# Optimization experiments

Measured on AMD Instinct MI355X. Metric: run time of the kernel, lower is better.

Reference implementation:

```python
import jax, jax.numpy as jnp
import numpy as np

N = 100000
E = 1600000
IN_F = 256
OUT_F = 128
ALPHA = 0.2  # LeakyReLU negative slope


def setup_inputs() -> dict:
    key = jax.random.key(0)
    k_x, k_e, k_w, k_al, k_ar = jax.random.split(key, 5)
    x = jax.random.normal(k_x, (N, IN_F), dtype=jnp.float32)
    edge_index = jax.random.randint(k_e, (2, E), 0, N, dtype=jnp.int64)
    # xavier_uniform with gain=1.414
    gain = 1.414
    lim_w = gain * np.sqrt(6.0 / (IN_F + OUT_F))
    W = jax.random.uniform(k_w, (IN_F, OUT_F), dtype=jnp.float32, minval=-lim_w, maxval=lim_w)
    lim_a = gain * np.sqrt(6.0 / (OUT_F + 1))
    a_left = jax.random.uniform(k_al, (OUT_F, 1), dtype=jnp.float32, minval=-lim_a, maxval=lim_a)
    a_right = jax.random.uniform(k_ar, (OUT_F, 1), dtype=jnp.float32, minval=-lim_a, maxval=lim_a)
    return {"x": x, "edge_index": edge_index, "W": W, "a_left": a_left, "a_right": a_right}


def reference(x, edge_index, W, a_left, a_right):
    src = edge_index[0]  # destination of aggregation (rows of adj)
    dst = edge_index[1]  # neighbor being attended to
    Wh = x @ W                              # [N, out_f]
    e_left = (Wh @ a_left)[:, 0]            # [N]
    e_right = (Wh @ a_right)[:, 0]          # [N]
    e = e_left[src] + e_right[dst]          # [E]
    e = jnp.where(e > 0, e, ALPHA * e)      # LeakyReLU
    # segment softmax over edges grouped by src node
    e_max = jax.ops.segment_max(e, src, num_segments=N)          # [N]
    e_exp = jnp.exp(e - e_max[src])                               # [E]
    e_sum = jax.ops.segment_sum(e_exp, src, num_segments=N)       # [N]
    alpha = e_exp / (e_sum[src] + 1e-9)                           # [E]
    messages = alpha[:, None] * Wh[dst]                           # [E, out_f]
    output = jax.ops.segment_sum(messages, src, num_segments=N)   # [N, out_f]
    return jax.nn.relu(output)
```

## Files before the change

### kernel.cpp

```cpp
#include <hip/hip_runtime.h>
#include <cstdint>
#include <cstddef>

static constexpr int IN_F  = 256;
static constexpr int OUT_F = 128;
#define ALPHA_SLOPE 0.2f
#define NB 256
#define BUCK_SH 7
#define CAP 6144

typedef __attribute__((ext_vector_type(8))) short short8;
typedef __attribute__((ext_vector_type(4))) float f32x4;
union ABFrag { uint32_t u[4]; short8 v; };

#define AS1 __attribute__((address_space(1)))
#define AS3 __attribute__((address_space(3)))

__device__ __forceinline__ uint32_t pack_bf2(float lo, float hi) {
    uint32_t ul = __float_as_uint(lo), uh = __float_as_uint(hi);
    uint32_t rl = (ul + 0x7fffu + ((ul >> 16) & 1u)) >> 16;
    uint32_t rh = (uh + 0x7fffu + ((uh >> 16) & 1u)) & 0xffff0000u;
    return rl | rh;
}
__device__ __forceinline__ uint32_t cvtpk_bf2(float lo, float hi) {
    uint32_t r;
    asm("v_cvt_pk_bf16_f32 %0, %1, %2" : "=v"(r) : "v"(lo), "v"(hi));
    return r;
}
__device__ __forceinline__ float blo(uint32_t w) { return __uint_as_float(w << 16); }
__device__ __forceinline__ float bhi(uint32_t w) { return __uint_as_float(w & 0xffff0000u); }

#define RL_F(x, l) __uint_as_float(__builtin_amdgcn_readlane(__float_as_uint(x), (l)))
#define RL_I(x, l) __builtin_amdgcn_readlane((x), (l))

__device__ __forceinline__ int edge_at(const void* ei, int idx, int is64) {
    return is64 ? (int)((const long long*)ei)[idx] : ((const int*)ei)[idx];
}

__global__ __launch_bounds__(256) void prep_hist_kernel(
    const float* __restrict__ W, const float* __restrict__ aL,
    const float* __restrict__ aR, const void* __restrict__ EI,
    int E, int nbuk, uint32_t* __restrict__ WtH,
    float* __restrict__ waL, float* __restrict__ waR, int* __restrict__ C)
{
    if (blockIdx.x < 64) {
        int dd = blockIdx.x * 256 + threadIdx.x;
        int n  = dd >> 7;
        int kd = (dd & 127) ^ ((n & 7) << 2);
        int k  = kd * 2;
        WtH[dd] = pack_bf2(W[(size_t)k * OUT_F + n], W[(size_t)(k + 1) * OUT_F + n]);
        return;
    }
    if (blockIdx.x == 64) {
        int k = threadIdx.x;
        const float* wr = W + (size_t)k * OUT_F;
        float sl = 0.f, sr = 0.f;
        for (int j = 0; j < OUT_F; j++) {
            float wv = wr[j];
            sl = fmaf(wv, aL[j], sl);
            sr = fmaf(wv, aR[j], sr);
        }
        waL[k] = sl; waR[k] = sr;
        return;
    }
    __shared__ int h[800];
    __shared__ int det;
    if (threadIdx.x == 0) det = 0;
    for (int b = threadIdx.x; b < nbuk; b += 256) h[b] = 0;
    __syncthreads();
    {
        const unsigned* eu = (const unsigned*)EI;
        int nz = 0;
        for (int i = threadIdx.x; i < 1024; i += 256)
            if (eu[2 * i + 1] != 0u) nz++;
        if (nz) atomicAdd(&det, 1);
    }
    __syncthreads();
    const int is64 = (det == 0);
    const int bid = blockIdx.x - 65;
    int chunk = (E + NB - 1) / NB;
    int start = bid * chunk;
    int end = min(start + chunk, E);
    for (int i = start + threadIdx.x; i < end; i += 256) {
        int s = edge_at(EI, i, is64);
        atomicAdd(&h[s >> BUCK_SH], 1);
    }
    __syncthreads();
    for (int b = threadIdx.x; b < nbuk; b += 256)
        C[b * NB + bid] = h[b];
}

__global__ __launch_bounds__(256) void scan1_kernel(const int* __restrict__ counts,
                                                    int* __restrict__ offsets,
                                                    int* __restrict__ partials, int N) {
    __shared__ int wt[4];
    int gid = blockIdx.x * 256 + threadIdx.x;
    const int lane = threadIdx.x & 63, wave = threadIdx.x >> 6;
    int c = (gid < N) ? counts[gid] : 0;
    int incl = c;
#pragma unroll
    for (int o = 1; o < 64; o <<= 1) {
        int v = __shfl_up(incl, o);
        if (lane >= o) incl += v;
    }
    if (lane == 63) wt[wave] = incl;
    __syncthreads();
    int woff = 0;
    for (int w = 0; w < wave; w++) woff += wt[w];
    if (gid < N) offsets[gid] = woff + incl - c;
    if (threadIdx.x == 0) partials[blockIdx.x] = wt[0] + wt[1] + wt[2] + wt[3];
}

__global__ __launch_bounds__(256) void scan2_kernel(int* data, int n) {
    __shared__ int wt[4];
    __shared__ int carry_s;
    if (threadIdx.x == 0) carry_s = 0;
    __syncthreads();
    const int lane = threadIdx.x & 63, wave = threadIdx.x >> 6;
    for (int base = 0; base < n; base += 256) {
        int i = base + threadIdx.x;
        int c = (i < n) ? data[i] : 0;
        int incl = c;
#pragma unroll
        for (int o = 1; o < 64; o <<= 1) {
            int v = __shfl_up(incl, o);
            if (lane >= o) incl += v;
        }
        if (lane == 63) wt[wave] = incl;
        __syncthreads();
        int woff = 0;
        for (int w = 0; w < wave; w++) woff += wt[w];
        int total = wt[0] + wt[1] + wt[2] + wt[3];
        int carry = carry_s;
        __syncthreads();
        if (i < n) data[i] = carry + woff + incl - c;
        if (threadIdx.x == 0) carry_s = carry + total;
        __syncthreads();
    }
}

__global__ __launch_bounds__(512, 4) void gemm_scatter_kernel(
    const float* __restrict__ X, const uint32_t* __restrict__ WtH,
    const float* __restrict__ waL, const float* __restrict__ waR,
    uint32_t* __restrict__ Whh, float* __restrict__ el, float* __restrict__ er,
    int M, const void* __restrict__ EI, int E, int nbuk,
    const int* __restrict__ Cx, const int* __restrict__ T,
    uint32_t* __restrict__ entries, int GB)
{
    __shared__ uint32_t ldsW[16384];
    __shared__ float    ldsWA[512];
    __shared__ int cur[800];
    __shared__ int det;
    const int tid = threadIdx.x;

    if (blockIdx.x >= GB) {
        if (tid == 0) det = 0;
        for (int b = tid; b < nbuk; b += 512) cur[b] = 0;
        __syncthreads();
        {
            const unsigned* eu = (const unsigned*)EI;
            int nz = 0;
            for (int i = tid; i < 1024; i += 512)
                if (eu[2 * i + 1] != 0u) nz++;
            if (nz) atomicAdd(&det, 1);
        }
        __syncthreads();
        const int is64 = (det == 0);
        const int bid = blockIdx.x - GB;
        int chunk = (E + NB - 1) / NB;
        int start = bid * chunk;
        int end = min(start + chunk, E);
        for (int i = start + tid; i < end; i += 512) {
            int s = edge_at(EI, i, is64);
            int d = edge_at(EI, E + i, is64);
            int b = s >> BUCK_SH;
            int pos = T[b] + Cx[b * NB + bid] + atomicAdd(&cur[b], 1);
            entries[pos] = ((uint32_t)(s & 127) << 17) | (uint32_t)d;
        }
        return;
    }

    const int w = tid >> 6, l = tid & 63;
    const int c = l & 15, kg = l >> 4;
    const int swz = (c & 7) << 2;

    const int bm = blockIdx.x * 128;
    const int myrow = w * 16 + c;
    const int grow = min(bm + myrow, M - 1);
    const bool rv = (bm + myrow) < M;
    const float* xp = X + (size_t)grow * IN_F + kg * 8;

    {
        const float* wsrc = (tid < 256) ? (waL + tid) : (waR + (tid - 256));
        __builtin_amdgcn_global_load_lds((AS1 const void*)wsrc,
                                         (AS3 void*)&ldsWA[tid], 4, 0, 0);
    }
    {
        const uint4* wsrc = (const uint4*)WtH;
        uint4* wdst = (uint4*)ldsW;
#pragma unroll
        for (int i = 0; i < 8; i++)
            __builtin_amdgcn_global_load_lds((AS1 const void*)(wsrc + tid + i * 512),
                                             (AS3 void*)(wdst + tid + i * 512), 16, 0, 0);
    }
    __builtin_amdgcn_sched_barrier(0);

    f32x4 xv[16];
#define GLOAD(DST, OFFS) \
    asm volatile("global_load_dwordx4 %0, %1, off offset:" OFFS : "=v"(DST) : "v"(xp))
    GLOAD(xv[0],  "0");   GLOAD(xv[1],  "16");
    GLOAD(xv[2],  "128"); GLOAD(xv[3],  "144");
    GLOAD(xv[4],  "256"); GLOAD(xv[5],  "272");
    GLOAD(xv[6],  "384"); GLOAD(xv[7],  "400");
    GLOAD(xv[8],  "512"); GLOAD(xv[9],  "528");
    GLOAD(xv[10], "640"); GLOAD(xv[11], "656");
    GLOAD(xv[12], "768"); GLOAD(xv[13], "784");
    GLOAD(xv[14], "896"); GLOAD(xv[15], "912");
#undef GLOAD
    __builtin_amdgcn_sched_barrier(0);

    f32x4 acc[8];
#pragma unroll
    for (int j = 0; j < 8; j++) acc[j] = (f32x4){0.f, 0.f, 0.f, 0.f};
    float sl = 0.f, sr = 0.f;

    asm volatile("s_waitcnt vmcnt(16)");
    __builtin_amdgcn_sched_barrier(0);
    __builtin_amdgcn_s_barrier();
    __builtin_amdgcn_sched_barrier(0);

#define GSTEP(KS, VMS)                                                        \
    {                                                                         \
        asm volatile("s_waitcnt vmcnt(" VMS ")");                             \
        __builtin_amdgcn_sched_barrier(0);                                    \
        f32x4 xa = xv[2 * KS], xb = xv[2 * KS + 1];                           \
        f32x4 l0 = *(const f32x4*)&ldsWA[KS * 32 + kg * 8];                   \
        f32x4 l1 = *(const f32x4*)&ldsWA[KS * 32 + kg * 8 + 4];               \
        f32x4 r0 = *(const f32x4*)&ldsWA[256 + KS * 32 + kg * 8];             \
        f32x4 r1 = *(const f32x4*)&ldsWA[256 + KS * 32 + kg * 8 + 4];         \
        _Pragma("unroll")                                                     \
        for (int i = 0; i < 4; i++) {                                         \
            sl = fmaf(xa[i], l0[i], sl); sl = fmaf(xb[i], l1[i], sl);         \
            sr = fmaf(xa[i], r0[i], sr); sr = fmaf(xb[i], r1[i], sr);         \
        }                                                                     \
        ABFrag a;                                                             \
        a.u[0] = cvtpk_bf2(xa[0], xa[1]); a.u[1] = cvtpk_bf2(xa[2], xa[3]);   \
        a.u[2] = cvtpk_bf2(xb[0], xb[1]); a.u[3] = cvtpk_bf2(xb[2], xb[3]);   \
        const int kd = KS * 16 + kg * 4;                                      \
        _Pragma("unroll")                                                     \
        for (int j = 0; j < 8; j++) {                                         \
            const int col = j * 16 + c;                                       \
            ABFrag b;                                                         \
            *(uint4*)b.u = *(const uint4*)&ldsW[col * 128 + (kd ^ swz)];      \
            acc[j] = __builtin_amdgcn_mfma_f32_16x16x32_bf16(a.v, b.v, acc[j], 0, 0, 0); \
        }                                                                     \
    }
    GSTEP(0, "14"); GSTEP(1, "12"); GSTEP(2, "10"); GSTEP(3, "8");
    GSTEP(4, "6");  GSTEP(5, "4");  GSTEP(6, "2");  GSTEP(7, "0");
#undef GSTEP

    sl += __shfl_xor(sl, 16); sl += __shfl_xor(sl, 32);
    sr += __shfl_xor(sr, 16); sr += __shfl_xor(sr, 32);
    if (rv && kg == 0) { el[bm + myrow] = sl; er[bm + myrow] = sr; }

    __syncthreads();
    float* sc = (float*)ldsW + w * 2048;
#pragma unroll
    for (int j = 0; j < 8; j++)
#pragma unroll
        for (int r = 0; r < 4; r++)
            sc[(kg * 4 + r) * 128 + j * 16 + c] = acc[j][r];
    __syncthreads();
#pragma unroll
    for (int m = 0; m < 16; m++) {
        float2 p = *(const float2*)&sc[m * 128 + 2 * l];
        int orow = bm + w * 16 + m;
        if (orow < M) Whh[(size_t)orow * 64 + l] = cvtpk_bf2(p.x, p.y);
    }
}

__global__ __launch_bounds__(256) void bucket_kernel(const uint32_t* __restrict__ entries,
                                                     const int* __restrict__ T,
                                                     int E, int N, int nbuk,
                                                     int* __restrict__ offsets,
                                                     int* __restrict__ edge_dst) {
    __shared__ uint32_t ent[CAP];
    __shared__ int outD[CAP];
    __shared__ int cnt[128], pre[128], cur[128];
    __shared__ int wt4[2];
    const int b = blockIdx.x;
    const int tid = threadIdx.x;
    const int base = T[b];
    const int cend = (b + 1 < nbuk) ? T[b + 1] : E;
    int count = cend - base;
    if (count > CAP) count = CAP;

    if (tid < 128) { cnt[tid] = 0; cur[tid] = 0; }
    __syncthreads();
    for (int k = tid; k < count; k += 256) {
        uint32_t e = entries[base + k];
        ent[k] = e;
        atomicAdd(&cnt[e >> 17], 1);
    }
    __syncthreads();
    {
        const int lane = tid & 63, w = tid >> 6;
        int c = (tid < 128) ? cnt[tid] : 0;
        int incl = c;
#pragma unroll
        for (int o = 1; o < 64; o <<= 1) {
            int v = __shfl_up(incl, o);
            if (lane >= o) incl += v;
        }
        if (w == 0 && lane == 63) wt4[0] = incl;
        __syncthreads();
        if (tid < 128) pre[tid] = ((w == 1) ? wt4[0] : 0) + incl - c;
        __syncthreads();
    }
    const int node0 = b << BUCK_SH;
    const int nnode = min(128, N - node0);
    if (tid < nnode) offsets[node0 + tid] = base + pre[tid];
    if (b == nbuk - 1 && tid == 0) offsets[N] = E;
    for (int k = tid; k < count; k += 256) {
        uint32_t e = ent[k];
        int sl = e >> 17;
        int p = pre[sl] + atomicAdd(&cur[sl], 1);
        outD[p] = (int)(e & 0x1FFFFu);
    }
    __syncthreads();
    for (int k = tid; k < count; k += 256)
        edge_dst[base + k] = outD[k];
}

__global__ __launch_bounds__(256) void node_kernel(const int* __restrict__ offsets,
                                                   const int* __restrict__ edge_dst,
                                                   const float* __restrict__ el,
                                                   const float* __restrict__ er,
                                                   const uint32_t* __restrict__ WhH,
                                                   float* __restrict__ out, int N) {
    int node = blockIdx.x * 4 + (threadIdx.x >> 6);
    int lane = threadIdx.x & 63;
    if (node >= N) return;
    int s0  = offsets[node];
    int deg = offsets[node + 1] - s0;
    float eli = el[node];

    if (deg <= 64) {
        int dj = 0;
        float e = -3.402823466e38f;
        if (lane < deg) {
            dj = edge_dst[s0 + lane];
            float t = eli + er[dj];
            e = t > 0.f ? t : ALPHA_SLOPE * t;
        }
        float m = e;
#pragma unroll
        for (int o = 32; o > 0; o >>= 1) m = fmaxf(m, __shfl_xor(m, o));
        float ex = (lane < deg) ? expf(e - m) : 0.f;
        float ssum = ex;
#pragma unroll
        for (int o = 32; o > 0; o >>= 1) ssum += __shfl_xor(ssum, o);
        float p = ex / (ssum + 1e-9f);

        const int g = lane >> 4, q = lane & 15;
        float a0 = 0.f, a1 = 0.f, a2 = 0.f, a3 = 0.f;
        float a4 = 0.f, a5 = 0.f, a6 = 0.f, a7 = 0.f;
        int rounds = (deg + 3) >> 2;
        int r = 0;
        for (; r + 4 <= rounds; r += 4) {
            int i0 = (r << 2) + g, i1 = i0 + 4, i2 = i0 + 8, i3 = i0 + 12;
            float p0 = __shfl(p, i0), p1 = __shfl(p, i1);
            float p2 = __shfl(p, i2), p3 = __shfl(p, i3);
            int   e0 = __shfl(dj, i0), e1 = __shfl(dj, i1);
            int   e2 = __shfl(dj, i2), e3 = __shfl(dj, i3);
            uint4 w0 = *(const uint4*)&WhH[(size_t)e0 * 64 + q * 4];
            uint4 w1 = *(const uint4*)&WhH[(size_t)e1 * 64 + q * 4];
            uint4 w2 = *(const uint4*)&WhH[(size_t)e2 * 64 + q * 4];
            uint4 w3 = *(const uint4*)&WhH[(size_t)e3 * 64 + q * 4];
            a0 = fmaf(p0, blo(w0.x), a0); a1 = fmaf(p0, bhi(w0.x), a1);
            a2 = fmaf(p0, blo(w0.y), a2); a3 = fmaf(p0, bhi(w0.y), a3);
            a4 = fmaf(p0, blo(w0.z), a4); a5 = fmaf(p0, bhi(w0.z), a5);
            a6 = fmaf(p0, blo(w0.w), a6); a7 = fmaf(p0, bhi(w0.w), a7);
            a0 = fmaf(p1, blo(w1.x), a0); a1 = fmaf(p1, bhi(w1.x), a1);
            a2 = fmaf(p1, blo(w1.y), a2); a3 = fmaf(p1, bhi(w1.y), a3);
            a4 = fmaf(p1, blo(w1.z), a4); a5 = fmaf(p1, bhi(w1.z), a5);
            a6 = fmaf(p1, blo(w1.w), a6); a7 = fmaf(p1, bhi(w1.w), a7);
            a0 = fmaf(p2, blo(w2.x), a0); a1 = fmaf(p2, bhi(w2.x), a1);
            a2 = fmaf(p2, blo(w2.y), a2); a3 = fmaf(p2, bhi(w2.y), a3);
            a4 = fmaf(p2, blo(w2.z), a4); a5 = fmaf(p2, bhi(w2.z), a5);
            a6 = fmaf(p2, blo(w2.w), a6); a7 = fmaf(p2, bhi(w2.w), a7);
            a0 = fmaf(p3, blo(w3.x), a0); a1 = fmaf(p3, bhi(w3.x), a1);
            a2 = fmaf(p3, blo(w3.y), a2); a3 = fmaf(p3, bhi(w3.y), a3);
            a4 = fmaf(p3, blo(w3.z), a4); a5 = fmaf(p3, bhi(w3.z), a5);
            a6 = fmaf(p3, blo(w3.w), a6); a7 = fmaf(p3, bhi(w3.w), a7);
        }
        for (; r + 2 <= rounds; r += 2) {
            int i0 = (r << 2) + g, i1 = i0 + 4;
            float p0 = __shfl(p, i0), p1 = __shfl(p, i1);
            int   e0 = __shfl(dj, i0), e1 = __shfl(dj, i1);
            uint4 w0 = *(const uint4*)&WhH[(size_t)e0 * 64 + q * 4];
            uint4 w1 = *(const uint4*)&WhH[(size_t)e1 * 64 + q * 4];
            a0 = fmaf(p0, blo(w0.x), a0); a1 = fmaf(p0, bhi(w0.x), a1);
            a2 = fmaf(p0, blo(w0.y), a2); a3 = fmaf(p0, bhi(w0.y), a3);
            a4 = fmaf(p0, blo(w0.z), a4); a5 = fmaf(p0, bhi(w0.z), a5);
            a6 = fmaf(p0, blo(w0.w), a6); a7 = fmaf(p0, bhi(w0.w), a7);
            a0 = fmaf(p1, blo(w1.x), a0); a1 = fmaf(p1, bhi(w1.x), a1);
            a2 = fmaf(p1, blo(w1.y), a2); a3 = fmaf(p1, bhi(w1.y), a3);
            a4 = fmaf(p1, blo(w1.z), a4); a5 = fmaf(p1, bhi(w1.z), a5);
            a6 = fmaf(p1, blo(w1.w), a6); a7 = fmaf(p1, bhi(w1.w), a7);
        }
        if (r < rounds) {
            int i0 = (r << 2) + g;
            float p0 = __shfl(p, i0);
            int   e0 = __shfl(dj, i0);
            uint4 w0 = *(const uint4*)&WhH[(size_t)e0 * 64 + q * 4];
            a0 = fmaf(p0, blo(w0.x), a0); a1 = fmaf(p0, bhi(w0.x), a1);
            a2 = fmaf(p0, blo(w0.y), a2); a3 = fmaf(p0, bhi(w0.y), a3);
            a4 = fmaf(p0, blo(w0.z), a4); a5 = fmaf(p0, bhi(w0.z), a5);
            a6 = fmaf(p0, blo(w0.w), a6); a7 = fmaf(p0, bhi(w0.w), a7);
        }
#pragma unroll
        for (int o = 16; o <= 32; o <<= 1) {
            a0 += __shfl_xor(a0, o); a1 += __shfl_xor(a1, o);
            a2 += __shfl_xor(a2, o); a3 += __shfl_xor(a3, o);
            a4 += __shfl_xor(a4, o); a5 += __shfl_xor(a5, o);
            a6 += __shfl_xor(a6, o); a7 += __shfl_xor(a7, o);
        }
        if (g == 0) {
            float4 o0 = make_float4(fmaxf(a0, 0.f), fmaxf(a1, 0.f),
                                    fmaxf(a2, 0.f), fmaxf(a3, 0.f));
            float4 o1 = make_float4(fmaxf(a4, 0.f), fmaxf(a5, 0.f),
                                    fmaxf(a6, 0.f), fmaxf(a7, 0.f));
            float* op = out + (size_t)node * OUT_F + q * 8;
            *(float4*)op = o0;
            *(float4*)(op + 4) = o1;
        }
        return;
    }

    float m = -3.402823466e38f;
    for (int j = lane; j < deg; j += 64) {
        float e = eli + er[edge_dst[s0 + j]];
        e = e > 0.f ? e : ALPHA_SLOPE * e;
        m = fmaxf(m, e);
    }
#pragma unroll
    for (int o = 32; o > 0; o >>= 1) m = fmaxf(m, __shfl_xor(m, o));

    float ssum = 0.f;
    for (int j = lane; j < deg; j += 64) {
        float e = eli + er[edge_dst[s0 + j]];
        e = e > 0.f ? e : ALPHA_SLOPE * e;
        ssum += expf(e - m);
    }
#pragma unroll
    for (int o = 32; o > 0; o >>= 1) ssum += __shfl_xor(ssum, o);
    float inv = 1.f / (ssum + 1e-9f);

    float acc0 = 0.f, acc1 = 0.f;
    for (int base = 0; base < deg; base += 64) {
        int j = base + lane;
        float p = 0.f;
        int d = 0;
        if (j < deg) {
            d = edge_dst[s0 + j];
            float e = eli + er[d];
            e = e > 0.f ? e : ALPHA_SLOPE * e;
            p = expf(e - m) * inv;
        }
        int cnt = min(64, deg - base);
        int t = 0;
        for (; t + 8 <= cnt; t += 8) {
            float b0 = RL_F(p, t + 0), b1 = RL_F(p, t + 1);
            float b2 = RL_F(p, t + 2), b3 = RL_F(p, t + 3);
            float b4 = RL_F(p, t + 4), b5 = RL_F(p, t + 5);
            float b6 = RL_F(p, t + 6), b7 = RL_F(p, t + 7);
            int   d0 = RL_I(d, t + 0), d1 = RL_I(d, t + 1);
            int   d2 = RL_I(d, t + 2), d3 = RL_I(d, t + 3);
            int   d4 = RL_I(d, t + 4), d5 = RL_I(d, t + 5);
            int   d6 = RL_I(d, t + 6), d7 = RL_I(d, t + 7);
            uint32_t w0 = WhH[(size_t)d0 * 64 + lane];
            uint32_t w1 = WhH[(size_t)d1 * 64 + lane];
            uint32_t w2 = WhH[(size_t)d2 * 64 + lane];
            uint32_t w3 = WhH[(size_t)d3 * 64 + lane];
            uint32_t w4 = WhH[(size_t)d4 * 64 + lane];
            uint32_t w5 = WhH[(size_t)d5 * 64 + lane];
            uint32_t w6 = WhH[(size_t)d6 * 64 + lane];
            uint32_t w7 = WhH[(size_t)d7 * 64 + lane];
            acc0 = fmaf(b0, blo(w0), acc0); acc1 = fmaf(b0, bhi(w0), acc1);
            acc0 = fmaf(b1, blo(w1), acc0); acc1 = fmaf(b1, bhi(w1), acc1);
            acc0 = fmaf(b2, blo(w2), acc0); acc1 = fmaf(b2, bhi(w2), acc1);
            acc0 = fmaf(b3, blo(w3), acc0); acc1 = fmaf(b3, bhi(w3), acc1);
            acc0 = fmaf(b4, blo(w4), acc0); acc1 = fmaf(b4, bhi(w4), acc1);
            acc0 = fmaf(b5, blo(w5), acc0); acc1 = fmaf(b5, bhi(w5), acc1);
            acc0 = fmaf(b6, blo(w6), acc0); acc1 = fmaf(b6, bhi(w6), acc1);
            acc0 = fmaf(b7, blo(w7), acc0); acc1 = fmaf(b7, bhi(w7), acc1);
        }
        for (; t < cnt; ++t) {
            float a = RL_F(p, t);
            int  dd = RL_I(d, t);
            uint32_t wv = WhH[(size_t)dd * 64 + lane];
            acc0 = fmaf(a, blo(wv), acc0);
            acc1 = fmaf(a, bhi(wv), acc1);
        }
    }
    out[(size_t)node * OUT_F + 2 * lane]     = fmaxf(acc0, 0.f);
    out[(size_t)node * OUT_F + 2 * lane + 1] = fmaxf(acc1, 0.f);
}

extern "C" void kernel_launch(void* const* d_in, const int* in_sizes, int n_in,
                              void* d_out, int out_size, void* d_ws, size_t ws_size,
                              hipStream_t stream) {
    (void)n_in; (void)out_size; (void)ws_size;
    const float* X  = (const float*)d_in[0];
    const void*  EI = d_in[1];
    const float* W  = (const float*)d_in[2];
    const float* aL = (const float*)d_in[3];
    const float* aR = (const float*)d_in[4];
    float* out = (float*)d_out;
    const int N = in_sizes[0] / IN_F;
    const int E = in_sizes[1] / 2;
    const int nbuk = (N + 127) >> BUCK_SH;
    const int GB = (N + 127) / 128;

    char* ws = (char*)d_ws;
    float*    waL      = (float*)(ws + 256);
    float*    waR      = waL + 256;
    uint32_t* WtH      = (uint32_t*)(waR + 256);
    uint32_t* Whh      = WtH + 16384;
    float*    el       = (float*)(Whh + (size_t)N * 64);
    float*    er       = el + N;
    int*      T        = (int*)(er + N);
    int*      C        = T + 1024;
    int*      Cx       = C + (size_t)nbuk * NB;
    int*      offsets  = Cx + (size_t)nbuk * NB;
    uint32_t* entries  = (uint32_t*)(offsets + (N + 1));
    int*      edge_dst = (int*)(entries + E);

    prep_hist_kernel<<<65 + NB, 256, 0, stream>>>(W, aL, aR, EI, E, nbuk,
                                                  WtH, waL, waR, C);
    scan1_kernel<<<nbuk, 256, 0, stream>>>(C, Cx, T, nbuk * NB);
    scan2_kernel<<<1, 256, 0, stream>>>(T, nbuk);
    gemm_scatter_kernel<<<GB + NB, 512, 0, stream>>>(X, WtH, waL, waR, Whh, el, er,
                                                     N, EI, E, nbuk, Cx, T,
                                                     entries, GB);
    bucket_kernel<<<nbuk, 256, 0, stream>>>(entries, T, E, N, nbuk, offsets, edge_dst);
    node_kernel<<<(N + 3) / 4, 256, 0, stream>>>(offsets, edge_dst, el, er, Whh, out, N);
}
```

Measured before the change: 151.7 us.

## Precast X to bf16 and compute attention logits in the scan kernel

```diff
diff --git a/kernel.cpp b/kernel.cpp
--- a/kernel.cpp
+++ b/kernel.cpp
@@ -90,25 +90,50 @@
         C[b * NB + bid] = h[b];
 }
 
-__global__ __launch_bounds__(256) void scan1_kernel(const int* __restrict__ counts,
-                                                    int* __restrict__ offsets,
-                                                    int* __restrict__ partials, int N) {
-    __shared__ int wt[4];
-    int gid = blockIdx.x * 256 + threadIdx.x;
-    const int lane = threadIdx.x & 63, wave = threadIdx.x >> 6;
-    int c = (gid < N) ? counts[gid] : 0;
-    int incl = c;
-#pragma unroll
-    for (int o = 1; o < 64; o <<= 1) {
-        int v = __shfl_up(incl, o);
-        if (lane >= o) incl += v;
-    }
-    if (lane == 63) wt[wave] = incl;
-    __syncthreads();
-    int woff = 0;
-    for (int w = 0; w < wave; w++) woff += wt[w];
-    if (gid < N) offsets[gid] = woff + incl - c;
-    if (threadIdx.x == 0) partials[blockIdx.x] = wt[0] + wt[1] + wt[2] + wt[3];
+__global__ __launch_bounds__(256) void scan1_xcast_kernel(
+    const int* __restrict__ counts, int* __restrict__ offsets,
+    int* __restrict__ partials, int NC,
+    const float* __restrict__ X, const float* __restrict__ waL,
+    const float* __restrict__ waR, uint32_t* __restrict__ Xh,
+    float* __restrict__ el, float* __restrict__ er, int N, int nbuk)
+{
+    if ((int)blockIdx.x < nbuk) {
+        __shared__ int wt[4];
+        int gid = blockIdx.x * 256 + threadIdx.x;
+        const int lane = threadIdx.x & 63, wave = threadIdx.x >> 6;
+        int c = (gid < NC) ? counts[gid] : 0;
+        int incl = c;
+#pragma unroll
+        for (int o = 1; o < 64; o <<= 1) {
+            int v = __shfl_up(incl, o);
+            if (lane >= o) incl += v;
+        }
+        if (lane == 63) wt[wave] = incl;
+        __syncthreads();
+        int woff = 0;
+        for (int w = 0; w < wave; w++) woff += wt[w];
+        if (gid < NC) offsets[gid] = woff + incl - c;
+        if (threadIdx.x == 0) partials[blockIdx.x] = wt[0] + wt[1] + wt[2] + wt[3];
+        return;
+    }
+    int row = ((int)blockIdx.x - nbuk) * 4 + (threadIdx.x >> 6);
+    int lane = threadIdx.x & 63;
+    if (row >= N) return;
+    float4 xv = *(const float4*)(X + (size_t)row * IN_F + lane * 4);
+    float4 l4 = *(const float4*)(waL + lane * 4);
+    float4 r4 = *(const float4*)(waR + lane * 4);
+    float sl = xv.x * l4.x + xv.y * l4.y + xv.z * l4.z + xv.w * l4.w;
+    float sr = xv.x * r4.x + xv.y * r4.y + xv.z * r4.z + xv.w * r4.w;
+#pragma unroll
+    for (int o = 32; o > 0; o >>= 1) {
+        sl += __shfl_xor(sl, o);
+        sr += __shfl_xor(sr, o);
+    }
+    uint2 pk;
+    pk.x = cvtpk_bf2(xv.x, xv.y);
+    pk.y = cvtpk_bf2(xv.z, xv.w);
+    *(uint2*)(Xh + (size_t)row * 128 + lane * 2) = pk;
+    if (lane == 0) { el[row] = sl; er[row] = sr; }
 }
 
 __global__ __launch_bounds__(256) void scan2_kernel(int* data, int n) {
@@ -139,16 +164,16 @@
     }
 }
 
-__global__ __launch_bounds__(512, 4) void gemm_scatter_kernel(
-    const float* __restrict__ X, const uint32_t* __restrict__ WtH,
-    const float* __restrict__ waL, const float* __restrict__ waR,
-    uint32_t* __restrict__ Whh, float* __restrict__ el, float* __restrict__ er,
-    int M, const void* __restrict__ EI, int E, int nbuk,
+__global__ __launch_bounds__(512)
+__attribute__((amdgpu_waves_per_eu(2, 4)))
+void gemm_scatter_kernel(
+    const uint32_t* __restrict__ Xh, const uint32_t* __restrict__ WtH,
+    uint32_t* __restrict__ Whh, int M,
+    const void* __restrict__ EI, int E, int nbuk,
     const int* __restrict__ Cx, const int* __restrict__ T,
     uint32_t* __restrict__ entries, int GB)
 {
     __shared__ uint32_t ldsW[16384];
-    __shared__ float    ldsWA[512];
     __shared__ int cur[800];
     __shared__ int det;
     const int tid = threadIdx.x;
@@ -187,14 +212,8 @@
     const int bm = blockIdx.x * 128;
     const int myrow = w * 16 + c;
     const int grow = min(bm + myrow, M - 1);
-    const bool rv = (bm + myrow) < M;
-    const float* xp = X + (size_t)grow * IN_F + kg * 8;
-
-    {
-        const float* wsrc = (tid < 256) ? (waL + tid) : (waR + (tid - 256));
-        __builtin_amdgcn_global_load_lds((AS1 const void*)wsrc,
-                                         (AS3 void*)&ldsWA[tid], 4, 0, 0);
-    }
+    const uint32_t* xp = Xh + (size_t)grow * 128 + kg * 4;
+
     {
         const uint4* wsrc = (const uint4*)WtH;
         uint4* wdst = (uint4*)ldsW;
@@ -205,26 +224,21 @@
     }
     __builtin_amdgcn_sched_barrier(0);
 
-    f32x4 xv[16];
+    uint4 xv[8];
 #define GLOAD(DST, OFFS) \
     asm volatile("global_load_dwordx4 %0, %1, off offset:" OFFS : "=v"(DST) : "v"(xp))
-    GLOAD(xv[0],  "0");   GLOAD(xv[1],  "16");
-    GLOAD(xv[2],  "128"); GLOAD(xv[3],  "144");
-    GLOAD(xv[4],  "256"); GLOAD(xv[5],  "272");
-    GLOAD(xv[6],  "384"); GLOAD(xv[7],  "400");
-    GLOAD(xv[8],  "512"); GLOAD(xv[9],  "528");
-    GLOAD(xv[10], "640"); GLOAD(xv[11], "656");
-    GLOAD(xv[12], "768"); GLOAD(xv[13], "784");
-    GLOAD(xv[14], "896"); GLOAD(xv[15], "912");
+    GLOAD(xv[0], "0");   GLOAD(xv[1], "64");
+    GLOAD(xv[2], "128"); GLOAD(xv[3], "192");
+    GLOAD(xv[4], "256"); GLOAD(xv[5], "320");
+    GLOAD(xv[6], "384"); GLOAD(xv[7], "448");
 #undef GLOAD
     __builtin_amdgcn_sched_barrier(0);
 
     f32x4 acc[8];
 #pragma unroll
     for (int j = 0; j < 8; j++) acc[j] = (f32x4){0.f, 0.f, 0.f, 0.f};
-    float sl = 0.f, sr = 0.f;
-
-    asm volatile("s_waitcnt vmcnt(16)");
+
+    asm volatile("s_waitcnt vmcnt(8)");
     __builtin_amdgcn_sched_barrier(0);
     __builtin_amdgcn_s_barrier();
     __builtin_amdgcn_sched_barrier(0);
@@ -233,19 +247,8 @@
     {                                                                         \
         asm volatile("s_waitcnt vmcnt(" VMS ")");                             \
         __builtin_amdgcn_sched_barrier(0);                                    \
-        f32x4 xa = xv[2 * KS], xb = xv[2 * KS + 1];                           \
-        f32x4 l0 = *(const f32x4*)&ldsWA[KS * 32 + kg * 8];                   \
-        f32x4 l1 = *(const f32x4*)&ldsWA[KS * 32 + kg * 8 + 4];               \
-        f32x4 r0 = *(const f32x4*)&ldsWA[256 + KS * 32 + kg * 8];             \
-        f32x4 r1 = *(const f32x4*)&ldsWA[256 + KS * 32 + kg * 8 + 4];         \
-        _Pragma("unroll")                                                     \
-        for (int i = 0; i < 4; i++) {                                         \
-            sl = fmaf(xa[i], l0[i], sl); sl = fmaf(xb[i], l1[i], sl);         \
-            sr = fmaf(xa[i], r0[i], sr); sr = fmaf(xb[i], r1[i], sr);         \
-        }                                                                     \
         ABFrag a;                                                             \
-        a.u[0] = cvtpk_bf2(xa[0], xa[1]); a.u[1] = cvtpk_bf2(xa[2], xa[3]);   \
-        a.u[2] = cvtpk_bf2(xb[0], xb[1]); a.u[3] = cvtpk_bf2(xb[2], xb[3]);   \
+        *(uint4*)a.u = xv[KS];                                                \
         const int kd = KS * 16 + kg * 4;                                      \
         _Pragma("unroll")                                                     \
         for (int j = 0; j < 8; j++) {                                         \
@@ -255,13 +258,9 @@
             acc[j] = __builtin_amdgcn_mfma_f32_16x16x32_bf16(a.v, b.v, acc[j], 0, 0, 0); \
         }                                                                     \
     }
-    GSTEP(0, "14"); GSTEP(1, "12"); GSTEP(2, "10"); GSTEP(3, "8");
-    GSTEP(4, "6");  GSTEP(5, "4");  GSTEP(6, "2");  GSTEP(7, "0");
+    GSTEP(0, "7"); GSTEP(1, "6"); GSTEP(2, "5"); GSTEP(3, "4");
+    GSTEP(4, "3"); GSTEP(5, "2"); GSTEP(6, "1"); GSTEP(7, "0");
 #undef GSTEP
-
-    sl += __shfl_xor(sl, 16); sl += __shfl_xor(sl, 32);
-    sr += __shfl_xor(sr, 16); sr += __shfl_xor(sr, 32);
-    if (rv && kg == 0) { el[bm + myrow] = sl; er[bm + myrow] = sr; }
 
     __syncthreads();
     float* sc = (float*)ldsW + w * 2048;
@@ -522,13 +521,15 @@
     const int E = in_sizes[1] / 2;
     const int nbuk = (N + 127) >> BUCK_SH;
     const int GB = (N + 127) / 128;
+    const int XB = (N + 3) / 4;
 
     char* ws = (char*)d_ws;
     float*    waL      = (float*)(ws + 256);
     float*    waR      = waL + 256;
     uint32_t* WtH      = (uint32_t*)(waR + 256);
     uint32_t* Whh      = WtH + 16384;
-    float*    el       = (float*)(Whh + (size_t)N * 64);
+    uint32_t* Xh       = Whh + (size_t)N * 64;
+    float*    el       = (float*)(Xh + (size_t)N * 128);
     float*    er       = el + N;
     int*      T        = (int*)(er + N);
     int*      C        = T + 1024;
@@ -539,10 +540,12 @@
 
     prep_hist_kernel<<<65 + NB, 256, 0, stream>>>(W, aL, aR, EI, E, nbuk,
                                                   WtH, waL, waR, C);
-    scan1_kernel<<<nbuk, 256, 0, stream>>>(C, Cx, T, nbuk * NB);
+    scan1_xcast_kernel<<<nbuk + XB, 256, 0, stream>>>(C, Cx, T, nbuk * NB,
+                                                      X, waL, waR, Xh, el, er,
+                                                      N, nbuk);
     scan2_kernel<<<1, 256, 0, stream>>>(T, nbuk);
-    gemm_scatter_kernel<<<GB + NB, 512, 0, stream>>>(X, WtH, waL, waR, Whh, el, er,
-                                                     N, EI, E, nbuk, Cx, T,
+    gemm_scatter_kernel<<<GB + NB, 512, 0, stream>>>(Xh, WtH, Whh, N,
+                                                     EI, E, nbuk, Cx, T,
                                                      entries, GB);
     bucket_kernel<<<nbuk, 256, 0, stream>>>(entries, T, E, N, nbuk, offsets, edge_dst);
     node_kernel<<<(N + 3) / 4, 256, 0, stream>>>(offsets, edge_dst, el, er, Whh, out, N);
```

New measurement: 182.8 us. 1.2x slower.

## Fuse bucket sort and per-node aggregation into one kernel using LDS adjacency

Applied to the files above, without the earlier changes.

```diff
diff --git a/kernel.cpp b/kernel.cpp
--- a/kernel.cpp
+++ b/kernel.cpp
@@ -29,9 +29,6 @@
 }
 __device__ __forceinline__ float blo(uint32_t w) { return __uint_as_float(w << 16); }
 __device__ __forceinline__ float bhi(uint32_t w) { return __uint_as_float(w & 0xffff0000u); }
-
-#define RL_F(x, l) __uint_as_float(__builtin_amdgcn_readlane(__float_as_uint(x), (l)))
-#define RL_I(x, l) __builtin_amdgcn_readlane((x), (l))
 
 __device__ __forceinline__ int edge_at(const void* ei, int idx, int is64) {
     return is64 ? (int)((const long long*)ei)[idx] : ((const int*)ei)[idx];
@@ -279,15 +276,15 @@
     }
 }
 
-__global__ __launch_bounds__(256) void bucket_kernel(const uint32_t* __restrict__ entries,
-                                                     const int* __restrict__ T,
-                                                     int E, int N, int nbuk,
-                                                     int* __restrict__ offsets,
-                                                     int* __restrict__ edge_dst) {
-    __shared__ uint32_t ent[CAP];
+__global__ __launch_bounds__(256) void bucket_node_kernel(
+    const uint32_t* __restrict__ entries, const int* __restrict__ T,
+    const float* __restrict__ el, const float* __restrict__ er,
+    const uint32_t* __restrict__ WhH, float* __restrict__ out,
+    int E, int N, int nbuk)
+{
     __shared__ int outD[CAP];
     __shared__ int cnt[128], pre[128], cur[128];
-    __shared__ int wt4[2];
+    __shared__ int wt4[1];
     const int b = blockIdx.x;
     const int tid = threadIdx.x;
     const int base = T[b];
@@ -297,11 +294,8 @@
 
     if (tid < 128) { cnt[tid] = 0; cur[tid] = 0; }
     __syncthreads();
-    for (int k = tid; k < count; k += 256) {
-        uint32_t e = entries[base + k];
-        ent[k] = e;
-        atomicAdd(&cnt[e >> 17], 1);
-    }
+    for (int k = tid; k < count; k += 256)
+        atomicAdd(&cnt[entries[base + k] >> 17], 1);
     __syncthreads();
     {
         const int lane = tid & 63, w = tid >> 6;
@@ -317,195 +311,159 @@
         if (tid < 128) pre[tid] = ((w == 1) ? wt4[0] : 0) + incl - c;
         __syncthreads();
     }
-    const int node0 = b << BUCK_SH;
-    const int nnode = min(128, N - node0);
-    if (tid < nnode) offsets[node0 + tid] = base + pre[tid];
-    if (b == nbuk - 1 && tid == 0) offsets[N] = E;
     for (int k = tid; k < count; k += 256) {
-        uint32_t e = ent[k];
+        uint32_t e = entries[base + k];
         int sl = e >> 17;
         int p = pre[sl] + atomicAdd(&cur[sl], 1);
         outD[p] = (int)(e & 0x1FFFFu);
     }
     __syncthreads();
-    for (int k = tid; k < count; k += 256)
-        edge_dst[base + k] = outD[k];
-}
-
-__global__ __launch_bounds__(256) void node_kernel(const int* __restrict__ offsets,
-                                                   const int* __restrict__ edge_dst,
-                                                   const float* __restrict__ el,
-                                                   const float* __restrict__ er,
-                                                   const uint32_t* __restrict__ WhH,
-                                                   float* __restrict__ out, int N) {
-    int node = blockIdx.x * 4 + (threadIdx.x >> 6);
-    int lane = threadIdx.x & 63;
-    if (node >= N) return;
-    int s0  = offsets[node];
-    int deg = offsets[node + 1] - s0;
-    float eli = el[node];
-
-    if (deg <= 64) {
-        int dj = 0;
-        float e = -3.402823466e38f;
-        if (lane < deg) {
-            dj = edge_dst[s0 + lane];
-            float t = eli + er[dj];
-            e = t > 0.f ? t : ALPHA_SLOPE * t;
-        }
-        float m = e;
+
+    const int node0 = b << BUCK_SH;
+    const int nnode = min(128, N - node0);
+    const int lane = tid & 63;
+    const int g = lane >> 4, q = lane & 15;
+
+    for (int nd = (tid >> 6); nd < nnode; nd += 4) {
+        const int node = node0 + nd;
+        const int s0 = pre[nd];
+        const int deg = cnt[nd];
+        const float eli = el[node];
+
+        if (deg <= 64) {
+            int dj = 0;
+            float e = -3.402823466e38f;
+            if (lane < deg) {
+                dj = outD[s0 + lane];
+                float t = eli + er[dj];
+                e = t > 0.f ? t : ALPHA_SLOPE * t;
+            }
+            float m = e;
+#pragma unroll
+            for (int o = 32; o > 0; o >>= 1) m = fmaxf(m, __shfl_xor(m, o));
+            float ex = (lane < deg) ? expf(e - m) : 0.f;
+            float ssum = ex;
+#pragma unroll
+            for (int o = 32; o > 0; o >>= 1) ssum += __shfl_xor(ssum, o);
+            float p = ex / (ssum + 1e-9f);
+
+            float a0 = 0.f, a1 = 0.f, a2 = 0.f, a3 = 0.f;
+            float a4 = 0.f, a5 = 0.f, a6 = 0.f, a7 = 0.f;
+            int rounds = (deg + 3) >> 2;
+            int r = 0;
+            for (; r + 4 <= rounds; r += 4) {
+                int i0 = (r << 2) + g, i1 = i0 + 4, i2 = i0 + 8, i3 = i0 + 12;
+                float p0 = __shfl(p, i0), p1 = __shfl(p, i1);
+                float p2 = __shfl(p, i2), p3 = __shfl(p, i3);
+                int   e0 = __shfl(dj, i0), e1 = __shfl(dj, i1);
+                int   e2 = __shfl(dj, i2), e3 = __shfl(dj, i3);
+                uint4 w0 = *(const uint4*)&WhH[(size_t)e0 * 64 + q * 4];
+                uint4 w1 = *(const uint4*)&WhH[(size_t)e1 * 64 + q * 4];
+                uint4 w2 = *(const uint4*)&WhH[(size_t)e2 * 64 + q * 4];
+                uint4 w3 = *(const uint4*)&WhH[(size_t)e3 * 64 + q * 4];
+                a0 = fmaf(p0, blo(w0.x), a0); a1 = fmaf(p0, bhi(w0.x), a1);
+                a2 = fmaf(p0, blo(w0.y), a2); a3 = fmaf(p0, bhi(w0.y), a3);
+                a4 = fmaf(p0, blo(w0.z), a4); a5 = fmaf(p0, bhi(w0.z), a5);
+                a6 = fmaf(p0, blo(w0.w), a6); a7 = fmaf(p0, bhi(w0.w), a7);
+                a0 = fmaf(p1, blo(w1.x), a0); a1 = fmaf(p1, bhi(w1.x), a1);
+                a2 = fmaf(p1, blo(w1.y), a2); a3 = fmaf(p1, bhi(w1.y), a3);
+                a4 = fmaf(p1, blo(w1.z), a4); a5 = fmaf(p1, bhi(w1.z), a5);
+                a6 = fmaf(p1, blo(w1.w), a6); a7 = fmaf(p1, bhi(w1.w), a7);
+                a0 = fmaf(p2, blo(w2.x), a0); a1 = fmaf(p2, bhi(w2.x), a1);
+                a2 = fmaf(p2, blo(w2.y), a2); a3 = fmaf(p2, bhi(w2.y), a3);
+                a4 = fmaf(p2, blo(w2.z), a4); a5 = fmaf(p2, bhi(w2.z), a5);
+                a6 = fmaf(p2, blo(w2.w), a6); a7 = fmaf(p2, bhi(w2.w), a7);
+                a0 = fmaf(p3, blo(w3.x), a0); a1 = fmaf(p3, bhi(w3.x), a1);
+                a2 = fmaf(p3, blo(w3.y), a2); a3 = fmaf(p3, bhi(w3.y), a3);
+                a4 = fmaf(p3, blo(w3.z), a4); a5 = fmaf(p3, bhi(w3.z), a5);
+                a6 = fmaf(p3, blo(w3.w), a6); a7 = fmaf(p3, bhi(w3.w), a7);
+            }
+            for (; r + 2 <= rounds; r += 2) {
+                int i0 = (r << 2) + g, i1 = i0 + 4;
+                float p0 = __shfl(p, i0), p1 = __shfl(p, i1);
+                int   e0 = __shfl(dj, i0), e1 = __shfl(dj, i1);
+                uint4 w0 = *(const uint4*)&WhH[(size_t)e0 * 64 + q * 4];
+                uint4 w1 = *(const uint4*)&WhH[(size_t)e1 * 64 + q * 4];
+                a0 = fmaf(p0, blo(w0.x), a0); a1 = fmaf(p0, bhi(w0.x), a1);
+                a2 = fmaf(p0, blo(w0.y), a2); a3 = fmaf(p0, bhi(w0.y), a3);
+                a4 = fmaf(p0, blo(w0.z), a4); a5 = fmaf(p0, bhi(w0.z), a5);
+                a6 = fmaf(p0, blo(w0.w), a6); a7 = fmaf(p0, bhi(w0.w), a7);
+                a0 = fmaf(p1, blo(w1.x), a0); a1 = fmaf(p1, bhi(w1.x), a1);
+                a2 = fmaf(p1, blo(w1.y), a2); a3 = fmaf(p1, bhi(w1.y), a3);
+                a4 = fmaf(p1, blo(w1.z), a4); a5 = fmaf(p1, bhi(w1.z), a5);
+                a6 = fmaf(p1, blo(w1.w), a6); a7 = fmaf(p1, bhi(w1.w), a7);
+            }
+            if (r < rounds) {
+                int i0 = (r << 2) + g;
+                float p0 = __shfl(p, i0);
+                int   e0 = __shfl(dj, i0);
+                uint4 w0 = *(const uint4*)&WhH[(size_t)e0 * 64 + q * 4];
+                a0 = fmaf(p0, blo(w0.x), a0); a1 = fmaf(p0, bhi(w0.x), a1);
+                a2 = fmaf(p0, blo(w0.y), a2); a3 = fmaf(p0, bhi(w0.y), a3);
+                a4 = fmaf(p0, blo(w0.z), a4); a5 = fmaf(p0, bhi(w0.z), a5);
+                a6 = fmaf(p0, blo(w0.w), a6); a7 = fmaf(p0, bhi(w0.w), a7);
+            }
+#pragma unroll
+            for (int o = 16; o <= 32; o <<= 1) {
+                a0 += __shfl_xor(a0, o); a1 += __shfl_xor(a1, o);
+                a2 += __shfl_xor(a2, o); a3 += __shfl_xor(a3, o);
+                a4 += __shfl_xor(a4, o); a5 += __shfl_xor(a5, o);
+                a6 += __shfl_xor(a6, o); a7 += __shfl_xor(a7, o);
+            }
+            if (g == 0) {
+                float4 o0 = make_float4(fmaxf(a0, 0.f), fmaxf(a1, 0.f),
+                                        fmaxf(a2, 0.f), fmaxf(a3, 0.f));
+                float4 o1 = make_float4(fmaxf(a4, 0.f), fmaxf(a5, 0.f),
+                                        fmaxf(a6, 0.f), fmaxf(a7, 0.f));
+                float* op = out + (size_t)node * OUT_F + q * 8;
+                *(float4*)op = o0;
+                *(float4*)(op + 4) = o1;
+            }
+            continue;
+        }
+
+        float m = -3.402823466e38f;
+        for (int j = lane; j < deg; j += 64) {
+            float e = eli + er[outD[s0 + j]];
+            e = e > 0.f ? e : ALPHA_SLOPE * e;
+            m = fmaxf(m, e);
+        }
 #pragma unroll
         for (int o = 32; o > 0; o >>= 1) m = fmaxf(m, __shfl_xor(m, o));
-        float ex = (lane < deg) ? expf(e - m) : 0.f;
-        float ssum = ex;
+
+        float ssum = 0.f;
+        for (int j = lane; j < deg; j += 64) {
+            float e = eli + er[outD[s0 + j]];
+            e = e > 0.f ? e : ALPHA_SLOPE * e;
+            ssum += expf(e - m);
+        }
 #pragma unroll
         for (int o = 32; o > 0; o >>= 1) ssum += __shfl_xor(ssum, o);
-        float p = ex / (ssum + 1e-9f);
-
-        const int g = lane >> 4, q = lane & 15;
-        float a0 = 0.f, a1 = 0.f, a2 = 0.f, a3 = 0.f;
-        float a4 = 0.f, a5 = 0.f, a6 = 0.f, a7 = 0.f;
-        int rounds = (deg + 3) >> 2;
-        int r = 0;
-        for (; r + 4 <= rounds; r += 4) {
-            int i0 = (r << 2) + g, i1 = i0 + 4, i2 = i0 + 8, i3 = i0 + 12;
-            float p0 = __shfl(p, i0), p1 = __shfl(p, i1);
-            float p2 = __shfl(p, i2), p3 = __shfl(p, i3);
-            int   e0 = __shfl(dj, i0), e1 = __shfl(dj, i1);
-            int   e2 = __shfl(dj, i2), e3 = __shfl(dj, i3);
-            uint4 w0 = *(const uint4*)&WhH[(size_t)e0 * 64 + q * 4];
-            uint4 w1 = *(const uint4*)&WhH[(size_t)e1 * 64 + q * 4];
-            uint4 w2 = *(const uint4*)&WhH[(size_t)e2 * 64 + q * 4];
-            uint4 w3 = *(const uint4*)&WhH[(size_t)e3 * 64 + q * 4];
-            a0 = fmaf(p0, blo(w0.x), a0); a1 = fmaf(p0, bhi(w0.x), a1);
-            a2 = fmaf(p0, blo(w0.y), a2); a3 = fmaf(p0, bhi(w0.y), a3);
-            a4 = fmaf(p0, blo(w0.z), a4); a5 = fmaf(p0, bhi(w0.z), a5);
-            a6 = fmaf(p0, blo(w0.w), a6); a7 = fmaf(p0, bhi(w0.w), a7);
-            a0 = fmaf(p1, blo(w1.x), a0); a1 = fmaf(p1, bhi(w1.x), a1);
-            a2 = fmaf(p1, blo(w1.y), a2); a3 = fmaf(p1, bhi(w1.y), a3);
-            a4 = fmaf(p1, blo(w1.z), a4); a5 = fmaf(p1, bhi(w1.z), a5);
-            a6 = fmaf(p1, blo(w1.w), a6); a7 = fmaf(p1, bhi(w1.w), a7);
-            a0 = fmaf(p2, blo(w2.x), a0); a1 = fmaf(p2, bhi(w2.x), a1);
-            a2 = fmaf(p2, blo(w2.y), a2); a3 = fmaf(p2, bhi(w2.y), a3);
-            a4 = fmaf(p2, blo(w2.z), a4); a5 = fmaf(p2, bhi(w2.z), a5);
-            a6 = fmaf(p2, blo(w2.w), a6); a7 = fmaf(p2, bhi(w2.w), a7);
-            a0 = fmaf(p3, blo(w3.x), a0); a1 = fmaf(p3, bhi(w3.x), a1);
-            a2 = fmaf(p3, blo(w3.y), a2); a3 = fmaf(p3, bhi(w3.y), a3);
-            a4 = fmaf(p3, blo(w3.z), a4); a5 = fmaf(p3, bhi(w3.z), a5);
-            a6 = fmaf(p3, blo(w3.w), a6); a7 = fmaf(p3, bhi(w3.w), a7);
-        }
-        for (; r + 2 <= rounds; r += 2) {
-            int i0 = (r << 2) + g, i1 = i0 + 4;
-            float p0 = __shfl(p, i0), p1 = __shfl(p, i1);
-            int   e0 = __shfl(dj, i0), e1 = __shfl(dj, i1);
-            uint4 w0 = *(const uint4*)&WhH[(size_t)e0 * 64 + q * 4];
-            uint4 w1 = *(const uint4*)&WhH[(size_t)e1 * 64 + q * 4];
-            a0 = fmaf(p0, blo(w0.x), a0); a1 = fmaf(p0, bhi(w0.x), a1);
-            a2 = fmaf(p0, blo(w0.y), a2); a3 = fmaf(p0, bhi(w0.y), a3);
-            a4 = fmaf(p0, blo(w0.z), a4); a5 = fmaf(p0, bhi(w0.z), a5);
-            a6 = fmaf(p0, blo(w0.w), a6); a7 = fmaf(p0, bhi(w0.w), a7);
-            a0 = fmaf(p1, blo(w1.x), a0); a1 = fmaf(p1, bhi(w1.x), a1);
-            a2 = fmaf(p1, blo(w1.y), a2); a3 = fmaf(p1, bhi(w1.y), a3);
-            a4 = fmaf(p1, blo(w1.z), a4); a5 = fmaf(p1, bhi(w1.z), a5);
-            a6 = fmaf(p1, blo(w1.w), a6); a7 = fmaf(p1, bhi(w1.w), a7);
-        }
-        if (r < rounds) {
-            int i0 = (r << 2) + g;
-            float p0 = __shfl(p, i0);
-            int   e0 = __shfl(dj, i0);
-            uint4 w0 = *(const uint4*)&WhH[(size_t)e0 * 64 + q * 4];
-            a0 = fmaf(p0, blo(w0.x), a0); a1 = fmaf(p0, bhi(w0.x), a1);
-            a2 = fmaf(p0, blo(w0.y), a2); a3 = fmaf(p0, bhi(w0.y), a3);
-            a4 = fmaf(p0, blo(w0.z), a4); a5 = fmaf(p0, bhi(w0.z), a5);
-            a6 = fmaf(p0, blo(w0.w), a6); a7 = fmaf(p0, bhi(w0.w), a7);
-        }
-#pragma unroll
-        for (int o = 16; o <= 32; o <<= 1) {
-            a0 += __shfl_xor(a0, o); a1 += __shfl_xor(a1, o);
-            a2 += __shfl_xor(a2, o); a3 += __shfl_xor(a3, o);
-            a4 += __shfl_xor(a4, o); a5 += __shfl_xor(a5, o);
-            a6 += __shfl_xor(a6, o); a7 += __shfl_xor(a7, o);
-        }
-        if (g == 0) {
-            float4 o0 = make_float4(fmaxf(a0, 0.f), fmaxf(a1, 0.f),
-                                    fmaxf(a2, 0.f), fmaxf(a3, 0.f));
-            float4 o1 = make_float4(fmaxf(a4, 0.f), fmaxf(a5, 0.f),
-                                    fmaxf(a6, 0.f), fmaxf(a7, 0.f));
-            float* op = out + (size_t)node * OUT_F + q * 8;
-            *(float4*)op = o0;
-            *(float4*)(op + 4) = o1;
-        }
-        return;
-    }
-
-    float m = -3.402823466e38f;
-    for (int j = lane; j < deg; j += 64) {
-        float e = eli + er[edge_dst[s0 + j]];
-        e = e > 0.f ? e : ALPHA_SLOPE * e;
-        m = fmaxf(m, e);
-    }
-#pragma unroll
-    for (int o = 32; o > 0; o >>= 1) m = fmaxf(m, __shfl_xor(m, o));
-
-    float ssum = 0.f;
-    for (int j = lane; j < deg; j += 64) {
-        float e = eli + er[edge_dst[s0 + j]];
-        e = e > 0.f ? e : ALPHA_SLOPE * e;
-        ssum += expf(e - m);
-    }
-#pragma unroll
-    for (int o = 32; o > 0; o >>= 1) ssum += __shfl_xor(ssum, o);
-    float inv = 1.f / (ssum + 1e-9f);
-
-    float acc0 = 0.f, acc1 = 0.f;
-    for (int base = 0; base < deg; base += 64) {
-        int j = base + lane;
-        float p = 0.f;
-        int d = 0;
-        if (j < deg) {
-            d = edge_dst[s0 + j];
-            float e = eli + er[d];
-            e = e > 0.f ? e : ALPHA_SLOPE * e;
-            p = expf(e - m) * inv;
-        }
-        int cnt = min(64, deg - base);
-        int t = 0;
-        for (; t + 8 <= cnt; t += 8) {
-            float b0 = RL_F(p, t + 0), b1 = RL_F(p, t + 1);
-            float b2 = RL_F(p, t + 2), b3 = RL_F(p, t + 3);
-            float b4 = RL_F(p, t + 4), b5 = RL_F(p, t + 5);
-            float b6 = RL_F(p, t + 6), b7 = RL_F(p, t + 7);
-            int   d0 = RL_I(d, t + 0), d1 = RL_I(d, t + 1);
-            int   d2 = RL_I(d, t + 2), d3 = RL_I(d, t + 3);
-            int   d4 = RL_I(d, t + 4), d5 = RL_I(d, t + 5);
-            int   d6 = RL_I(d, t + 6), d7 = RL_I(d, t + 7);
-            uint32_t w0 = WhH[(size_t)d0 * 64 + lane];
-            uint32_t w1 = WhH[(size_t)d1 * 64 + lane];
-            uint32_t w2 = WhH[(size_t)d2 * 64 + lane];
-            uint32_t w3 = WhH[(size_t)d3 * 64 + lane];
-            uint32_t w4 = WhH[(size_t)d4 * 64 + lane];
-            uint32_t w5 = WhH[(size_t)d5 * 64 + lane];
-            uint32_t w6 = WhH[(size_t)d6 * 64 + lane];
-            uint32_t w7 = WhH[(size_t)d7 * 64 + lane];
-            acc0 = fmaf(b0, blo(w0), acc0); acc1 = fmaf(b0, bhi(w0), acc1);
-            acc0 = fmaf(b1, blo(w1), acc0); acc1 = fmaf(b1, bhi(w1), acc1);
-            acc0 = fmaf(b2, blo(w2), acc0); acc1 = fmaf(b2, bhi(w2), acc1);
-            acc0 = fmaf(b3, blo(w3), acc0); acc1 = fmaf(b3, bhi(w3), acc1);
-            acc0 = fmaf(b4, blo(w4), acc0); acc1 = fmaf(b4, bhi(w4), acc1);
-            acc0 = fmaf(b5, blo(w5), acc0); acc1 = fmaf(b5, bhi(w5), acc1);
-            acc0 = fmaf(b6, blo(w6), acc0); acc1 = fmaf(b6, bhi(w6), acc1);
-            acc0 = fmaf(b7, blo(w7), acc0); acc1 = fmaf(b7, bhi(w7), acc1);
-        }
-        for (; t < cnt; ++t) {
-            float a = RL_F(p, t);
-            int  dd = RL_I(d, t);
-            uint32_t wv = WhH[(size_t)dd * 64 + lane];
-            acc0 = fmaf(a, blo(wv), acc0);
-            acc1 = fmaf(a, bhi(wv), acc1);
-        }
-    }
-    out[(size_t)node * OUT_F + 2 * lane]     = fmaxf(acc0, 0.f);
-    out[(size_t)node * OUT_F + 2 * lane + 1] = fmaxf(acc1, 0.f);
+        float inv = 1.f / (ssum + 1e-9f);
+
+        float acc0 = 0.f, acc1 = 0.f;
+        for (int bb = 0; bb < deg; bb += 64) {
+            int j = bb + lane;
+            float p = 0.f;
+            int d = 0;
+            if (j < deg) {
+                d = outD[s0 + j];
+                float e = eli + er[d];
+                e = e > 0.f ? e : ALPHA_SLOPE * e;
+                p = expf(e - m) * inv;
+            }
+            int cnt2 = min(64, deg - bb);
+            for (int t = 0; t < cnt2; ++t) {
+                float a = __uint_as_float(__builtin_amdgcn_readlane(__float_as_uint(p), t));
+                int  dd = __builtin_amdgcn_readlane(d, t);
+                uint32_t wv = WhH[(size_t)dd * 64 + lane];
+                acc0 = fmaf(a, blo(wv), acc0);
+                acc1 = fmaf(a, bhi(wv), acc1);
+            }
+        }
+        out[(size_t)node * OUT_F + 2 * lane]     = fmaxf(acc0, 0.f);
+        out[(size_t)node * OUT_F + 2 * lane + 1] = fmaxf(acc1, 0.f);
+    }
 }
 
 extern "C" void kernel_launch(void* const* d_in, const int* in_sizes, int n_in,
@@ -533,9 +491,7 @@
     int*      T        = (int*)(er + N);
     int*      C        = T + 1024;
     int*      Cx       = C + (size_t)nbuk * NB;
-    int*      offsets  = Cx + (size_t)nbuk * NB;
-    uint32_t* entries  = (uint32_t*)(offsets + (N + 1));
-    int*      edge_dst = (int*)(entries + E);
+    uint32_t* entries  = (uint32_t*)(Cx + (size_t)nbuk * NB);
 
     prep_hist_kernel<<<65 + NB, 256, 0, stream>>>(W, aL, aR, EI, E, nbuk,
                                                   WtH, waL, waR, C);
@@ -544,6 +500,6 @@
     gemm_scatter_kernel<<<GB + NB, 512, 0, stream>>>(X, WtH, waL, waR, Whh, el, er,
                                                      N, EI, E, nbuk, Cx, T,
                                                      entries, GB);
-    bucket_kernel<<<nbuk, 256, 0, stream>>>(entries, T, E, N, nbuk, offsets, edge_dst);
-    node_kernel<<<(N + 3) / 4, 256, 0, stream>>>(offsets, edge_dst, el, er, Whh, out, N);
-}
+    bucket_node_kernel<<<nbuk, 256, 0, stream>>>(entries, T, el, er, Whh, out,
+                                                 E, N, nbuk);
+}
```

After: 153.1 us. Within noise of the previous version (+0.9%).
